# Kernel tuning notes

Hardware: AMD Instinct MI355X
Metric: run time of the kernel (lower is better)

The kernel has to match this reference:

```python
import jax, jax.numpy as jnp
import numpy as np

B, N, C, H = 2048, 15, 1024, 16
HS = C // H  # 64
SCALE = HS ** -0.5
EPS = 1e-5


def _ln(x, g, b):
    m = jnp.mean(x, axis=-1, keepdims=True)
    v = jnp.mean(jnp.square(x - m), axis=-1, keepdims=True)
    return (x - m) * jax.lax.rsqrt(v + EPS) * g + b


def setup_inputs() -> dict:
    key = jax.random.key(0)
    ks = jax.random.split(key, 20)
    s = lambda fan_in: 1.0 / np.sqrt(fan_in)
    inp = {
        "joint_feature": jax.random.normal(ks[0], (B, N, C), jnp.float32),
        "relation_feature": jax.random.normal(ks[1], (B, N, C), jnp.float32),
        # weights stored as [in, out] (transposed vs torch Linear)
        "W_Jqkv": jax.random.uniform(ks[2], (C, 3 * C), jnp.float32, -s(C), s(C)),
        "W_Iqk": jax.random.uniform(ks[3], (C, 3 * C), jnp.float32, -s(C), s(C)),
        "W_Iconv": jax.random.uniform(ks[4], (HS, 15), jnp.float32, -s(HS), s(HS)),
        "W_proj": jax.random.uniform(ks[5], (C, C), jnp.float32, -s(C), s(C)),
        "b_proj": jax.random.uniform(ks[6], (C,), jnp.float32, -s(C), s(C)),
        "g_attn1": jnp.ones((C,), jnp.float32),
        "b_attn1": jnp.zeros((C,), jnp.float32),
        "g_attn2": jnp.ones((C,), jnp.float32),
        "b_attn2": jnp.zeros((C,), jnp.float32),
        "g_joint": jnp.ones((C,), jnp.float32),
        "b_joint": jnp.zeros((C,), jnp.float32),
        "W_fc1": jax.random.uniform(ks[7], (C, C // 2), jnp.float32, -s(C), s(C)),
        "b_fc1": jax.random.uniform(ks[8], (C // 2,), jnp.float32, -s(C), s(C)),
        "W_fc2": jax.random.uniform(ks[9], (C // 2, C), jnp.float32, -s(C // 2), s(C // 2)),
        "b_fc2": jax.random.uniform(ks[10], (C,), jnp.float32, -s(C // 2), s(C // 2)),
    }
    return inp


def reference(joint_feature, relation_feature, W_Jqkv, W_Iqk, W_Iconv, W_proj, b_proj,
              g_attn1, b_attn1, g_attn2, b_attn2, g_joint, b_joint,
              W_fc1, b_fc1, W_fc2, b_fc2):
    # --- Attention_I on normalized streams ---
    xj = _ln(joint_feature, g_attn1, b_attn1)      # [B,N,C]
    xi = _ln(relation_feature, g_attn2, b_attn2)   # [B,N,C]

    Jqkv = (xj @ W_Jqkv).reshape(B, N, 3, H, HS).transpose(2, 0, 3, 1, 4)  # [3,B,H,N,HS]
    Jq, Jk, Jv = Jqkv[0], Jqkv[1], Jqkv[2]
    Iqkv = (xi @ W_Iqk).reshape(B, N, 3, H, HS).transpose(2, 0, 3, 1, 4)
    Iq, Ik, Iv = Iqkv[0], Iqkv[1], Iqkv[2]

    attn_J = jnp.einsum("bhqd,bhkd->bhqk", Jq, Jk)
    attn_I = jnp.einsum("bhqd,bhkd->bhqk", Iq, Ik)
    attn_lin = Iv @ W_Iconv                        # [B,H,N,15] == [B,H,N,N]
    attn = jax.nn.softmax((attn_J + attn_I + attn_lin) * SCALE, axis=-1)

    x = jnp.einsum("bhqk,bhkd->bhqd", attn, Jv)    # [B,H,N,HS]
    x = x.transpose(0, 2, 1, 3).reshape(B, N, C)
    x = x @ W_proj + b_proj

    joint = joint_feature + x

    # --- MLP (hidden = dim // 2) ---
    y = _ln(joint, g_joint, b_joint)
    y = jax.nn.gelu(y @ W_fc1 + b_fc1, approximate=False)
    y = y @ W_fc2 + b_fc2
    return joint + y
```

## Files before the change

kernel.cpp:

```cpp
#include <hip/hip_runtime.h>
#include <math.h>


typedef __attribute__((ext_vector_type(8))) short short8;
typedef __attribute__((ext_vector_type(4))) float fx4;

#define MROWS 30720

#define GLL16(g, l)                                                         \
    __builtin_amdgcn_global_load_lds(                                       \
        (const __attribute__((address_space(1))) unsigned int*)(g),         \
        (__attribute__((address_space(3))) unsigned int*)(l), 16, 0, 0)

__device__ inline unsigned short f2bf(float f) {
    unsigned int u = __float_as_uint(f);
    unsigned int r = (u + 0x7fffu + ((u >> 16) & 1u)) >> 16;
    return (unsigned short)r;
}
__device__ inline float bf2f(unsigned short s) {
    return __uint_as_float(((unsigned int)s) << 16);
}

__global__ __launch_bounds__(256) void transpose_w(const float* __restrict__ W,
                                                   unsigned short* __restrict__ Wt,
                                                   int K, int N) {
    __shared__ float tile[32][33];
    int bn = blockIdx.x * 32;
    int bk = blockIdx.y * 32;
    int tx = threadIdx.x & 31, ty = threadIdx.x >> 5;
    #pragma unroll
    for (int i = ty; i < 32; i += 8)
        tile[i][tx] = W[(size_t)(bk + i) * N + bn + tx];
    __syncthreads();
    #pragma unroll
    for (int i = ty; i < 32; i += 8)
        Wt[(size_t)(bn + i) * K + bk + tx] = f2bf(tile[tx][i]);
}

__global__ __launch_bounds__(256) void ln_dual(const float* __restrict__ xa,
                                               const float* __restrict__ ga,
                                               const float* __restrict__ bba,
                                               unsigned short* __restrict__ oa,
                                               const float* __restrict__ xb,
                                               const float* __restrict__ gb,
                                               const float* __restrict__ bbb,
                                               unsigned short* __restrict__ ob) {
    const float* x = blockIdx.y ? xb : xa;
    const float* g = blockIdx.y ? gb : ga;
    const float* bv = blockIdx.y ? bbb : bba;
    unsigned short* out = blockIdx.y ? ob : oa;

    int row = blockIdx.x;
    int t = threadIdx.x;
    const float4* xp = (const float4*)(x + (size_t)row * 1024);
    float4 v = xp[t];
    float s  = v.x + v.y + v.z + v.w;
    float ss = v.x * v.x + v.y * v.y + v.z * v.z + v.w * v.w;
    #pragma unroll
    for (int o = 32; o > 0; o >>= 1) { s += __shfl_down(s, o); ss += __shfl_down(ss, o); }
    __shared__ float ps[4], pss[4], stat[2];
    int wv = t >> 6, ln = t & 63;
    if (ln == 0) { ps[wv] = s; pss[wv] = ss; }
    __syncthreads();
    if (t == 0) {
        float S = ps[0] + ps[1] + ps[2] + ps[3];
        float SS = pss[0] + pss[1] + pss[2] + pss[3];
        float m = S * (1.0f / 1024.0f);
        float var = SS * (1.0f / 1024.0f) - m * m;
        stat[0] = m; stat[1] = rsqrtf(var + 1e-5f);
    }
    __syncthreads();
    float m = stat[0], r = stat[1];
    float4 gg = ((const float4*)g)[t];
    float4 bb = ((const float4*)bv)[t];
    ushort4 o;
    o.x = f2bf((v.x - m) * r * gg.x + bb.x);
    o.y = f2bf((v.y - m) * r * gg.y + bb.y);
    o.z = f2bf((v.z - m) * r * gg.z + bb.z);
    o.w = f2bf((v.w - m) * r * gg.w + bb.w);
    ((ushort4*)(out + (size_t)row * 1024))[t] = o;
}

template <int EPI, int K>
__global__ __launch_bounds__(256) void gemm_lds(const unsigned short* __restrict__ A,
                                                const unsigned short* __restrict__ Bt,
                                                const unsigned short* __restrict__ A2,
                                                const unsigned short* __restrict__ Bt2,
                                                const float* __restrict__ bias,
                                                const float* __restrict__ resid,
                                                float* __restrict__ outF,
                                                unsigned short* __restrict__ outB,
                                                unsigned short* __restrict__ outB2,
                                                int N) {
    if (EPI == 0 && blockIdx.z) { A = A2; Bt = Bt2; outB = outB2; }

    __shared__ unsigned short lA[128 * 32];
    __shared__ unsigned short lB[128 * 32];

    const int t = threadIdx.x;
    const int wave = t >> 6, lane = t & 63;
    const int rowf = lane & 15, quad = lane >> 4;

    const int m0 = blockIdx.y * 128;
    const int n0 = blockIdx.x * 128;
    const int wm0 = (wave >> 1) * 64;
    const int wn0 = (wave & 1) * 64;

    const int srow = t >> 2;
    const int skc  = (t & 3) * 8;
    const unsigned short* gA0 = A  + (size_t)(m0 + srow) * K + skc;
    const unsigned short* gA1 = A  + (size_t)(m0 + srow + 64) * K + skc;
    const unsigned short* gB0 = Bt + (size_t)(n0 + srow) * K + skc;
    const unsigned short* gB1 = Bt + (size_t)(n0 + srow + 64) * K + skc;
    unsigned short* dA0 = lA + (size_t)t * 8;
    unsigned short* dA1 = lA + (size_t)(t + 256) * 8;
    unsigned short* dB0 = lB + (size_t)t * 8;
    unsigned short* dB1 = lB + (size_t)(t + 256) * 8;

    fx4 acc[4][4] = {};

    for (int k0 = 0; k0 < K; k0 += 32) {
        GLL16(gA0, dA0); GLL16(gA1, dA1);
        GLL16(gB0, dB0); GLL16(gB1, dB1);
        gA0 += 32; gA1 += 32; gB0 += 32; gB1 += 32;
        __syncthreads();

        short8 a[4], b[4];
        #pragma unroll
        for (int i = 0; i < 4; i++)
            a[i] = *(const short8*)(lA + (wm0 + 16 * i + rowf) * 32 + quad * 8);
        #pragma unroll
        for (int j = 0; j < 4; j++)
            b[j] = *(const short8*)(lB + (wn0 + 16 * j + rowf) * 32 + quad * 8);
        #pragma unroll
        for (int i = 0; i < 4; i++)
            #pragma unroll
            for (int j = 0; j < 4; j++)
                acc[i][j] = __builtin_amdgcn_mfma_f32_16x16x32_bf16(a[i], b[j], acc[i][j], 0, 0, 0);
        __syncthreads();
    }

    #pragma unroll
    for (int i = 0; i < 4; i++) {
        #pragma unroll
        for (int j = 0; j < 4; j++) {
            int col = n0 + wn0 + 16 * j + rowf;
            #pragma unroll
            for (int r = 0; r < 4; r++) {
                int row = m0 + wm0 + 16 * i + quad * 4 + r;
                size_t off = (size_t)row * N + col;
                float v = acc[i][j][r];
                if (EPI == 0) {
                    outB[off] = f2bf(v);
                } else if (EPI == 1) {
                    outF[off] = v + bias[col] + resid[off];
                } else {
                    v += bias[col];
                    v = 0.5f * v * (1.0f + erff(v * 0.70710678118654752f));
                    outB[off] = f2bf(v);
                }
            }
        }
    }
}

__global__ __launch_bounds__(256) void attn_kernel(const unsigned short* __restrict__ Jqkv,
                                                   const unsigned short* __restrict__ Iqkv,
                                                   const float* __restrict__ Wc,
                                                   unsigned short* __restrict__ xout) {
    int b = blockIdx.x >> 4;
    int h = blockIdx.x & 15;
    __shared__ float J[3][15][65];
    __shared__ float I[3][15][65];
    __shared__ float W[64][17];
    __shared__ float P[15][16];

    const unsigned short* Jb = Jqkv + (size_t)b * 15 * 3072 + h * 64;
    const unsigned short* Ib = Iqkv + (size_t)b * 15 * 3072 + h * 64;

    for (int idx = threadIdx.x; idx < 15 * 3 * 64; idx += 256) {
        int n = idx / 192, rem = idx % 192;
        int r = rem / 64, d = rem % 64;
        J[r][n][d] = bf2f(Jb[(size_t)n * 3072 + r * 1024 + d]);
        I[r][n][d] = bf2f(Ib[(size_t)n * 3072 + r * 1024 + d]);
    }
    for (int idx = threadIdx.x; idx < 64 * 15; idx += 256)
        W[idx / 15][idx % 15] = Wc[idx];
    __syncthreads();

    for (int idx = threadIdx.x; idx < 225; idx += 256) {
        int q = idx / 15, kk = idx % 15;
        float s = 0.0f;
        #pragma unroll 8
        for (int d = 0; d < 64; d++)
            s += J[0][q][d] * J[1][kk][d] + I[0][q][d] * I[1][kk][d] + I[2][q][d] * W[d][kk];
        P[q][kk] = s * 0.125f;
    }
    __syncthreads();

    if (threadIdx.x < 15) {
        int q = threadIdx.x;
        float mx = -1e30f;
        #pragma unroll
        for (int kk = 0; kk < 15; kk++) mx = fmaxf(mx, P[q][kk]);
        float e[15], sum = 0.0f;
        #pragma unroll
        for (int kk = 0; kk < 15; kk++) { e[kk] = __expf(P[q][kk] - mx); sum += e[kk]; }
        float inv = 1.0f / sum;
        #pragma unroll
        for (int kk = 0; kk < 15; kk++) P[q][kk] = e[kk] * inv;
    }
    __syncthreads();

    for (int idx = threadIdx.x; idx < 960; idx += 256) {
        int q = idx >> 6, d = idx & 63;
        float o = 0.0f;
        #pragma unroll
        for (int kk = 0; kk < 15; kk++) o += P[q][kk] * J[2][kk][d];
        xout[((size_t)b * 15 + q) * 1024 + h * 64 + d] = f2bf(o);
    }
}

extern "C" void kernel_launch(void* const* d_in, const int* in_sizes, int n_in,
                              void* d_out, int out_size, void* d_ws, size_t ws_size,
                              hipStream_t stream) {
    const float* joint_feature    = (const float*)d_in[0];
    const float* relation_feature = (const float*)d_in[1];
    const float* W_Jqkv  = (const float*)d_in[2];
    const float* W_Iqk   = (const float*)d_in[3];
    const float* W_Iconv = (const float*)d_in[4];
    const float* W_proj  = (const float*)d_in[5];
    const float* b_proj  = (const float*)d_in[6];
    const float* g1  = (const float*)d_in[7];
    const float* be1 = (const float*)d_in[8];
    const float* g2  = (const float*)d_in[9];
    const float* be2 = (const float*)d_in[10];
    const float* gj  = (const float*)d_in[11];
    const float* bj  = (const float*)d_in[12];
    const float* W_fc1 = (const float*)d_in[13];
    const float* b_fc1 = (const float*)d_in[14];
    const float* W_fc2 = (const float*)d_in[15];
    const float* b_fc2 = (const float*)d_in[16];

    char* ws = (char*)d_ws;
    unsigned short* WtJ  = (unsigned short*)(ws + 0);
    unsigned short* WtI  = (unsigned short*)(ws + 6291456);
    unsigned short* WtP  = (unsigned short*)(ws + 12582912);
    unsigned short* WtF1 = (unsigned short*)(ws + 14680064);
    unsigned short* WtF2 = (unsigned short*)(ws + 15728640);
    unsigned short* xj   = (unsigned short*)(ws + 16777216);
    unsigned short* xi   = (unsigned short*)(ws + 79691776);
    unsigned short* xattn = (unsigned short*)(ws + 142606336);
    float*          joint = (float*)(ws + 16777216);
    unsigned short* yln   = xattn;
    unsigned short* h1    = (unsigned short*)(ws + 205520896);
    int CH = 16;
    {
        const int opts[5] = {1, 2, 4, 8, 16};
        for (int i = 0; i < 5; i++) {
            size_t need = 205520896ull + 754974720ull / (size_t)opts[i];
            if (need <= ws_size) { CH = opts[i]; break; }
        }
    }
    const int Mc = MROWS / CH;
    const size_t chunkBytes = 754974720ull / (size_t)CH / 2ull;
    unsigned short* Jqkv_c = (unsigned short*)(ws + 205520896);
    unsigned short* Iqkv_c = (unsigned short*)(ws + 205520896 + chunkBytes);

    dim3 blk(256);

    transpose_w<<<dim3(96, 32), blk, 0, stream>>>(W_Jqkv, WtJ, 1024, 3072);
    transpose_w<<<dim3(96, 32), blk, 0, stream>>>(W_Iqk,  WtI, 1024, 3072);
    transpose_w<<<dim3(32, 32), blk, 0, stream>>>(W_proj, WtP, 1024, 1024);
    transpose_w<<<dim3(16, 32), blk, 0, stream>>>(W_fc1, WtF1, 1024, 512);
    transpose_w<<<dim3(32, 16), blk, 0, stream>>>(W_fc2, WtF2, 512, 1024);

    ln_dual<<<dim3(MROWS, 2), blk, 0, stream>>>(joint_feature, g1, be1, xj,
                                                relation_feature, g2, be2, xi);

    for (int c = 0; c < CH; c++) {
        size_t ro = (size_t)c * Mc * 1024;
        gemm_lds<0, 1024><<<dim3(24, Mc / 128, 2), blk, 0, stream>>>(
            xj + ro, WtJ, xi + ro, WtI, nullptr, nullptr, nullptr, Jqkv_c, Iqkv_c, 3072);
        attn_kernel<<<(Mc / 15) * 16, blk, 0, stream>>>(Jqkv_c, Iqkv_c, W_Iconv, xattn + ro);
    }

    gemm_lds<1, 1024><<<dim3(8, 240), blk, 0, stream>>>(
        xattn, WtP, nullptr, nullptr, b_proj, joint_feature, joint, nullptr, nullptr, 1024);

    ln_dual<<<dim3(MROWS, 1), blk, 0, stream>>>(joint, gj, bj, yln,
                                                nullptr, nullptr, nullptr, nullptr);

    gemm_lds<2, 1024><<<dim3(4, 240), blk, 0, stream>>>(
        yln, WtF1, nullptr, nullptr, b_fc1, nullptr, nullptr, h1, nullptr, 512);

    gemm_lds<1, 512><<<dim3(8, 240), blk, 0, stream>>>(
        h1, WtF2, nullptr, nullptr, b_fc2, joint, (float*)d_out, nullptr, nullptr, 1024);
}
```

Baseline: 1.444 ms.

## Double-buffer GEMM LDS tiles, remap blocks across XCDs, vectorize epilogues and attention IO

```diff
diff --git a/kernel.cpp b/kernel.cpp
--- a/kernel.cpp
+++ b/kernel.cpp
@@ -3,6 +3,7 @@
 
 
 typedef __attribute__((ext_vector_type(8))) short short8;
+typedef __attribute__((ext_vector_type(8))) unsigned short ush8;
 typedef __attribute__((ext_vector_type(4))) float fx4;
 
 #define MROWS 30720
@@ -94,71 +95,118 @@
                                                 int N) {
     if (EPI == 0 && blockIdx.z) { A = A2; Bt = Bt2; outB = outB2; }
 
-    __shared__ unsigned short lA[128 * 32];
-    __shared__ unsigned short lB[128 * 32];
-
-    const int t = threadIdx.x;
-    const int wave = t >> 6, lane = t & 63;
+    __shared__ __align__(16) char smem[32768];
+    unsigned short* lA = (unsigned short*)smem;
+    unsigned short* lB = (unsigned short*)(smem + 16384);
+
+    const int tid = threadIdx.x;
+    const int wave = tid >> 6, lane = tid & 63;
     const int rowf = lane & 15, quad = lane >> 4;
 
-    const int m0 = blockIdx.y * 128;
-    const int n0 = blockIdx.x * 128;
+    int bx = blockIdx.x, by = blockIdx.y;
+    if (gridDim.x <= 8) {
+        int nwg = gridDim.x * gridDim.y;
+        int lid = by * gridDim.x + bx;
+        int q = nwg >> 3, r = nwg & 7;
+        int xcd = lid & 7, pos = lid >> 3;
+        int nl = (xcd < r ? xcd * (q + 1) : r * (q + 1) + (xcd - r) * q) + pos;
+        bx = nl % gridDim.x;
+        by = nl / gridDim.x;
+    }
+
+    const int m0 = by * 128;
+    const int n0 = bx * 128;
     const int wm0 = (wave >> 1) * 64;
     const int wn0 = (wave & 1) * 64;
 
-    const int srow = t >> 2;
-    const int skc  = (t & 3) * 8;
+    const int srow = tid >> 2;
+    const int skc  = (tid & 3) * 8;
     const unsigned short* gA0 = A  + (size_t)(m0 + srow) * K + skc;
     const unsigned short* gA1 = A  + (size_t)(m0 + srow + 64) * K + skc;
     const unsigned short* gB0 = Bt + (size_t)(n0 + srow) * K + skc;
     const unsigned short* gB1 = Bt + (size_t)(n0 + srow + 64) * K + skc;
-    unsigned short* dA0 = lA + (size_t)t * 8;
-    unsigned short* dA1 = lA + (size_t)(t + 256) * 8;
-    unsigned short* dB0 = lB + (size_t)t * 8;
-    unsigned short* dB1 = lB + (size_t)(t + 256) * 8;
 
     fx4 acc[4][4] = {};
 
-    for (int k0 = 0; k0 < K; k0 += 32) {
-        GLL16(gA0, dA0); GLL16(gA1, dA1);
-        GLL16(gB0, dB0); GLL16(gB1, dB1);
-        gA0 += 32; gA1 += 32; gB0 += 32; gB1 += 32;
-        __syncthreads();
-
+    const int NT = K / 32;
+
+    GLL16(gA0, lA + (size_t)tid * 8);
+    GLL16(gA1, lA + (size_t)(tid + 256) * 8);
+    GLL16(gB0, lB + (size_t)tid * 8);
+    GLL16(gB1, lB + (size_t)(tid + 256) * 8);
+    gA0 += 32; gA1 += 32; gB0 += 32; gB1 += 32;
+    __syncthreads();
+
+    #pragma unroll 2
+    for (int t = 0; t < NT; ++t) {
+        const int cur = t & 1, nxt = cur ^ 1;
+        if (t + 1 < NT) {
+            GLL16(gA0, lA + nxt * 4096 + (size_t)tid * 8);
+            GLL16(gA1, lA + nxt * 4096 + (size_t)(tid + 256) * 8);
+            GLL16(gB0, lB + nxt * 4096 + (size_t)tid * 8);
+            GLL16(gB1, lB + nxt * 4096 + (size_t)(tid + 256) * 8);
+            gA0 += 32; gA1 += 32; gB0 += 32; gB1 += 32;
+        }
+        const unsigned short* sA = lA + cur * 4096;
+        const unsigned short* sB = lB + cur * 4096;
         short8 a[4], b[4];
         #pragma unroll
         for (int i = 0; i < 4; i++)
-            a[i] = *(const short8*)(lA + (wm0 + 16 * i + rowf) * 32 + quad * 8);
+            a[i] = *(const short8*)(sA + (wm0 + 16 * i + rowf) * 32 + quad * 8);
         #pragma unroll
         for (int j = 0; j < 4; j++)
-            b[j] = *(const short8*)(lB + (wn0 + 16 * j + rowf) * 32 + quad * 8);
+            b[j] = *(const short8*)(sB + (wn0 + 16 * j + rowf) * 32 + quad * 8);
         #pragma unroll
         for (int i = 0; i < 4; i++)
             #pragma unroll
             for (int j = 0; j < 4; j++)
                 acc[i][j] = __builtin_amdgcn_mfma_f32_16x16x32_bf16(a[i], b[j], acc[i][j], 0, 0, 0);
-        __syncthreads();
-    }
+        asm volatile("s_waitcnt vmcnt(0) lgkmcnt(0)\n\ts_barrier" ::: "memory");
+    }
+
+    float* st = (float*)smem + wave * 1280;
+    const int rl  = lane >> 2;
+    const int c0l = (lane & 3) * 16;
+    const int colb = n0 + wn0 + c0l;
 
     #pragma unroll
     for (int i = 0; i < 4; i++) {
         #pragma unroll
-        for (int j = 0; j < 4; j++) {
-            int col = n0 + wn0 + 16 * j + rowf;
+        for (int j = 0; j < 4; j++)
             #pragma unroll
-            for (int r = 0; r < 4; r++) {
-                int row = m0 + wm0 + 16 * i + quad * 4 + r;
-                size_t off = (size_t)row * N + col;
-                float v = acc[i][j][r];
-                if (EPI == 0) {
-                    outB[off] = f2bf(v);
-                } else if (EPI == 1) {
-                    outF[off] = v + bias[col] + resid[off];
-                } else {
-                    v += bias[col];
-                    v = 0.5f * v * (1.0f + erff(v * 0.70710678118654752f));
-                    outB[off] = f2bf(v);
+            for (int r = 0; r < 4; r++)
+                st[(quad * 4 + r) * 80 + 16 * j + rowf] = acc[i][j][r];
+        const int row = m0 + wm0 + 16 * i + rl;
+        if (EPI == 1) {
+            #pragma unroll
+            for (int kk = 0; kk < 4; kk++) {
+                float4 v  = *(const float4*)(st + rl * 80 + c0l + 4 * kk);
+                float4 bb = *((const float4*)(bias + colb) + kk);
+                float4 rr = *((const float4*)(resid + (size_t)row * N + colb) + kk);
+                v.x += bb.x + rr.x; v.y += bb.y + rr.y;
+                v.z += bb.z + rr.z; v.w += bb.w + rr.w;
+                *((float4*)(outF + (size_t)row * N + colb) + kk) = v;
+            }
+        } else {
+            #pragma unroll
+            for (int h = 0; h < 2; h++) {
+                float4 va = *(const float4*)(st + rl * 80 + c0l + 8 * h);
+                float4 vb = *(const float4*)(st + rl * 80 + c0l + 8 * h + 4);
+                float f[8] = {va.x, va.y, va.z, va.w, vb.x, vb.y, vb.z, vb.w};
+                if (EPI == 2) {
+                    float4 ba = *((const float4*)(bias + colb) + 2 * h);
+                    float4 bc = *((const float4*)(bias + colb) + 2 * h + 1);
+                    float bf[8] = {ba.x, ba.y, ba.z, ba.w, bc.x, bc.y, bc.z, bc.w};
+                    #pragma unroll
+                    for (int e = 0; e < 8; e++) {
+                        float v = f[e] + bf[e];
+                        f[e] = 0.5f * v * (1.0f + erff(v * 0.70710678118654752f));
+                    }
                 }
+                ush8 o;
+                #pragma unroll
+                for (int e = 0; e < 8; e++) o[e] = f2bf(f[e]);
+                *(ush8*)(outB + (size_t)row * N + colb + 8 * h) = o;
             }
         }
     }
@@ -178,11 +226,16 @@
     const unsigned short* Jb = Jqkv + (size_t)b * 15 * 3072 + h * 64;
     const unsigned short* Ib = Iqkv + (size_t)b * 15 * 3072 + h * 64;
 
-    for (int idx = threadIdx.x; idx < 15 * 3 * 64; idx += 256) {
-        int n = idx / 192, rem = idx % 192;
-        int r = rem / 64, d = rem % 64;
-        J[r][n][d] = bf2f(Jb[(size_t)n * 3072 + r * 1024 + d]);
-        I[r][n][d] = bf2f(Ib[(size_t)n * 3072 + r * 1024 + d]);
+    for (int idx = threadIdx.x; idx < 360; idx += 256) {
+        int n = idx / 24, rem = idx % 24;
+        int r = rem >> 3, d0 = (rem & 7) * 8;
+        short8 vj = *(const short8*)(Jb + (size_t)n * 3072 + r * 1024 + d0);
+        short8 vi = *(const short8*)(Ib + (size_t)n * 3072 + r * 1024 + d0);
+        #pragma unroll
+        for (int e = 0; e < 8; e++) {
+            J[r][n][d0 + e] = bf2f((unsigned short)vj[e]);
+            I[r][n][d0 + e] = bf2f((unsigned short)vi[e]);
+        }
     }
     for (int idx = threadIdx.x; idx < 64 * 15; idx += 256)
         W[idx / 15][idx % 15] = Wc[idx];
@@ -212,12 +265,20 @@
     }
     __syncthreads();
 
-    for (int idx = threadIdx.x; idx < 960; idx += 256) {
-        int q = idx >> 6, d = idx & 63;
-        float o = 0.0f;
-        #pragma unroll
-        for (int kk = 0; kk < 15; kk++) o += P[q][kk] * J[2][kk][d];
-        xout[((size_t)b * 15 + q) * 1024 + h * 64 + d] = f2bf(o);
+    for (int idx = threadIdx.x; idx < 240; idx += 256) {
+        int q = idx >> 4, d0 = (idx & 15) * 4;
+        float o0 = 0.0f, o1 = 0.0f, o2 = 0.0f, o3 = 0.0f;
+        #pragma unroll
+        for (int kk = 0; kk < 15; kk++) {
+            float p = P[q][kk];
+            o0 += p * J[2][kk][d0 + 0];
+            o1 += p * J[2][kk][d0 + 1];
+            o2 += p * J[2][kk][d0 + 2];
+            o3 += p * J[2][kk][d0 + 3];
+        }
+        ushort4 o;
+        o.x = f2bf(o0); o.y = f2bf(o1); o.z = f2bf(o2); o.w = f2bf(o3);
+        *(ushort4*)(xout + ((size_t)b * 15 + q) * 1024 + h * 64 + d0) = o;
     }
 }
 
```

New measurement: 1.456 ms. About the same (+0.8%).
